# Kernel optimization log

Measured on AMD Instinct MI355X. Metric: run time of the kernel, lower is better.

The kernel has to match this reference:

```python
import jax, jax.numpy as jnp
import numpy as np

B, S, D, H = 4, 2048, 1024, 16
DH = D // H
SCALE = float(np.sqrt(DH))


def setup_inputs() -> dict:
    key = jax.random.key(0)
    ks = jax.random.split(key, 5)
    std = 1.0 / np.sqrt(D)
    return {
        "x": jax.random.normal(ks[0], (B, S, D), dtype=jnp.float32),
        "Wq": jax.random.normal(ks[1], (D, D), dtype=jnp.float32) * std,
        "bq": jnp.zeros((D,), dtype=jnp.float32),
        "Wk": jax.random.normal(ks[2], (D, D), dtype=jnp.float32) * std,
        "bk": jnp.zeros((D,), dtype=jnp.float32),
        "Wv": jax.random.normal(ks[3], (D, D), dtype=jnp.float32) * std,
        "bv": jnp.zeros((D,), dtype=jnp.float32),
        "Wo": jax.random.normal(ks[4], (D, D), dtype=jnp.float32) * std,
        "bo": jnp.zeros((D,), dtype=jnp.float32),
        "padding_mask": jnp.ones((B, S), dtype=jnp.int32),
    }


def reference(x, Wq, bq, Wk, bk, Wv, bv, Wo, bo, padding_mask):
    b, s, d = x.shape
    # QKV projections, split heads -> [b, h, s, dh]
    q = (x @ Wq + bq).reshape(b, s, H, DH).transpose(0, 2, 1, 3)
    k = (x @ Wk + bk).reshape(b, s, H, DH).transpose(0, 2, 1, 3)
    v = (x @ Wv + bv).reshape(b, s, H, DH).transpose(0, 2, 1, 3)
    # scaled scores [b, h, s, s]
    scores = jnp.einsum('bhqd,bhkd->bhqk', q, k) / SCALE
    neg_inf = jnp.float32(-jnp.inf)
    causal = jnp.tril(jnp.ones((s, s), dtype=bool))  # [s, s]
    scores = jnp.where(causal[None, None, :, :], scores, neg_inf)
    pad = (padding_mask != 0)[:, None, None, :]  # [b,1,1,s] on key axis
    scores = jnp.where(pad, scores, neg_inf)
    weights = jax.nn.softmax(scores, axis=-1)
    weights = jnp.nan_to_num(weights, nan=0.0)  # fully-masked rows -> 0
    # dropout is identity in eval / p=0
    attended = jnp.einsum('bhqk,bhkd->bhqd', weights, v)
    attended = attended.transpose(0, 2, 1, 3).reshape(b, s, d)
    return attended @ Wo + bo
```

## Files before the change

### kernel.cpp

```cpp
#include <hip/hip_runtime.h>
#include <hip/hip_bf16.h>

#define B_   4
#define S_   2048
#define D_   1024
#define H_   16
#define DH_  64
#define M_   (B_ * S_)

typedef __attribute__((ext_vector_type(8))) short  bfrag8;
typedef __attribute__((ext_vector_type(4))) float  facc4;
typedef unsigned short u16;
typedef unsigned long long u64;

__device__ __forceinline__ u16 f2bf(float f) {
    union { __hip_bfloat16 h; u16 u; } c;
    c.h = __float2bfloat16(f);
    return c.u;
}

__device__ __forceinline__ u16 bfr(float f) {
    unsigned b = __float_as_uint(f);
    return (u16)((b + 0x7FFFu + ((b >> 16) & 1u)) >> 16);
}

__device__ __forceinline__ void gl_lds16(const u16* g, u16* l) {
    __builtin_amdgcn_global_load_lds((const __attribute__((address_space(1))) void*)g,
                                     (__attribute__((address_space(3))) void*)l,
                                     16, 0, 0);
}

__global__ __launch_bounds__(256) void cvt_x(const float* __restrict__ x,
                                             u16* __restrict__ o, int n) {
    int i = (blockIdx.x * 256 + threadIdx.x) * 4;
    if (i >= n) return;
    float4 v = *(const float4*)(x + i);
    ushort4 r;
    r.x = f2bf(v.x); r.y = f2bf(v.y); r.z = f2bf(v.z); r.w = f2bf(v.w);
    *(ushort4*)(o + i) = r;
}

__global__ __launch_bounds__(256) void cvt_wt(const float* __restrict__ w0, const float* __restrict__ w1,
                                              const float* __restrict__ w2, const float* __restrict__ w3,
                                              u16* __restrict__ o0, u16* __restrict__ o1,
                                              u16* __restrict__ o2, u16* __restrict__ o3) {
    const float* w; u16* o;
    switch (blockIdx.z) {
        case 0: w = w0; o = o0; break;
        case 1: w = w1; o = o1; break;
        case 2: w = w2; o = o2; break;
        default: w = w3; o = o3; break;
    }
    __shared__ u16 t[32][33];
    int kb = blockIdx.x * 32, nb = blockIdx.y * 32;
    int c = threadIdx.x & 31, r0 = threadIdx.x >> 5;
#pragma unroll
    for (int i = 0; i < 4; i++) {
        int r = r0 + 8 * i;
        t[r][c] = f2bf(w[(kb + r) * D_ + nb + c]);
    }
    __syncthreads();
#pragma unroll
    for (int i = 0; i < 4; i++) {
        int r = r0 + 8 * i;
        o[(nb + r) * D_ + kb + c] = t[c][r];
    }
}

__global__ __launch_bounds__(64) void pack_pm(const int* __restrict__ pm,
                                              unsigned* __restrict__ pmw) {
    int b = blockIdx.x, lane = threadIdx.x;
#pragma unroll
    for (int j = 0; j < 32; ++j) {
        u64 m = __ballot(pm[b * S_ + j * 64 + lane] != 0);
        if (lane == 0) {
            pmw[b * 64 + 2 * j]     = (unsigned)m;
            pmw[b * 64 + 2 * j + 1] = (unsigned)(m >> 32);
        }
    }
}

__device__ __forceinline__ void gemm_body(const u16* __restrict__ A,
                                          const u16* __restrict__ BT,
                                          const float* __restrict__ bias,
                                          void* __restrict__ Cout, int mode, float scale,
                                          u16* As, u16* Bs) {
    int tid = threadIdx.x;
    int nb = blockIdx.x * 128, mb = blockIdx.y * 128;
    int w = tid >> 6, lane = tid & 63, quad = lane >> 4, l16 = lane & 15;
    int wm = (w >> 1) * 64, wn = (w & 1) * 64;

    int c0 = tid, c1 = tid + 256;
    int row0 = c0 >> 2, row1 = c1 >> 2;
    int sw0 = (c0 & 3) ^ ((row0 >> 2) & 3);
    int sw1 = (c1 & 3) ^ ((row1 >> 2) & 3);
    const u16* Ag0 = A + (mb + row0) * D_ + sw0 * 8;
    const u16* Ag1 = A + (mb + row1) * D_ + sw1 * 8;
    const u16* Bg0 = BT + (nb + row0) * D_ + sw0 * 8;
    const u16* Bg1 = BT + (nb + row1) * D_ + sw1 * 8;
    u16* Al0 = As + c0 * 8; u16* Al1 = As + c1 * 8;
    u16* Bl0 = Bs + c0 * 8; u16* Bl1 = Bs + c1 * 8;

    int swr = (l16 >> 2) & 3;

    facc4 acc[4][4] = {};
    for (int kk = 0; kk < D_; kk += 32) {
        __syncthreads();
        gl_lds16(Ag0 + kk, Al0);
        gl_lds16(Ag1 + kk, Al1);
        gl_lds16(Bg0 + kk, Bl0);
        gl_lds16(Bg1 + kk, Bl1);
        __syncthreads();

        bfrag8 af[4], bf[4];
#pragma unroll
        for (int mt = 0; mt < 4; ++mt)
            af[mt] = *(const bfrag8*)(As + (wm + mt * 16 + l16) * 32 + ((quad ^ swr) << 3));
#pragma unroll
        for (int nt = 0; nt < 4; ++nt)
            bf[nt] = *(const bfrag8*)(Bs + (wn + nt * 16 + l16) * 32 + ((quad ^ swr) << 3));
#pragma unroll
        for (int mt = 0; mt < 4; ++mt)
#pragma unroll
            for (int nt = 0; nt < 4; ++nt)
                acc[mt][nt] = __builtin_amdgcn_mfma_f32_16x16x32_bf16(af[mt], bf[nt], acc[mt][nt], 0, 0, 0);
    }

#pragma unroll
    for (int mt = 0; mt < 4; ++mt) {
        int m_base = mb + wm + mt * 16 + quad * 4;
#pragma unroll
        for (int nt = 0; nt < 4; ++nt) {
            int n = nb + wn + nt * 16 + l16;
            float bv = bias[n];
            int h = n >> 6, dd = n & 63;
#pragma unroll
            for (int r = 0; r < 4; ++r) {
                int m = m_base + r;
                float v = (acc[mt][nt][r] + bv) * scale;
                int bi = m >> 11, s = m & (S_ - 1);
                if (mode == 0) {
                    ((u16*)Cout)[(((bi * H_ + h) * S_) + s) * DH_ + dd] = bfr(v);
                } else if (mode == 1) {
                    ((u16*)Cout)[(((bi * H_ + h) * DH_) + dd) * S_ + s] = bfr(v);
                } else {
                    ((float*)Cout)[(size_t)m * D_ + n] = v;
                }
            }
        }
    }
}

#define CE_Q 0.18033688011112042f

__global__ __launch_bounds__(256) void gemm_qkv(const u16* __restrict__ A,
                                                const u16* __restrict__ WTq, const float* __restrict__ bq, u16* __restrict__ Qb,
                                                const u16* __restrict__ WTk, const float* __restrict__ bk, u16* __restrict__ Kb,
                                                const u16* __restrict__ WTv, const float* __restrict__ bv, u16* __restrict__ VTb) {
    __shared__ u16 As[128 * 32];
    __shared__ u16 Bs[128 * 32];
    switch (blockIdx.z) {
        case 0: gemm_body(A, WTq, bq, Qb, 0, CE_Q, As, Bs); break;
        case 1: gemm_body(A, WTk, bk, Kb, 0, 1.0f, As, Bs); break;
        default: gemm_body(A, WTv, bv, VTb, 1, 1.0f, As, Bs); break;
    }
}

__global__ __launch_bounds__(256) void gemm_o(const u16* __restrict__ A,
                                              const u16* __restrict__ WTo, const float* __restrict__ bo,
                                              float* __restrict__ out) {
    __shared__ u16 As[128 * 32];
    __shared__ u16 Bs[128 * 32];
    gemm_body(A, WTo, bo, out, 2, 1.0f, As, Bs);
}

__device__ __forceinline__ void soft_pv(const float* p, float& lp, facc4* oaccq,
                                        const bfrag8* vf, int a0, int a1, bool qlo) {
    float rs = 0.f;
    unsigned pk[4];
#pragma unroll
    for (int j = 0; j < 4; ++j) {
        float e0 = exp2f(p[2 * j]);
        float e1 = exp2f(p[2 * j + 1]);
        rs += e0; rs += e1;
        pk[j] = __builtin_amdgcn_perm(__float_as_uint(e1), __float_as_uint(e0), 0x07060302u);
    }
    lp += rs;
    union { unsigned d[4]; bfrag8 v; } pb;
    {
        unsigned lo, hi;
        lo = __builtin_amdgcn_ds_bpermute(a0, (int)pk[0]);
        hi = __builtin_amdgcn_ds_bpermute(a0, (int)pk[2]);
        pb.d[0] = qlo ? lo : hi;
        lo = __builtin_amdgcn_ds_bpermute(a0, (int)pk[1]);
        hi = __builtin_amdgcn_ds_bpermute(a0, (int)pk[3]);
        pb.d[1] = qlo ? lo : hi;
        lo = __builtin_amdgcn_ds_bpermute(a1, (int)pk[0]);
        hi = __builtin_amdgcn_ds_bpermute(a1, (int)pk[2]);
        pb.d[2] = qlo ? lo : hi;
        lo = __builtin_amdgcn_ds_bpermute(a1, (int)pk[1]);
        hi = __builtin_amdgcn_ds_bpermute(a1, (int)pk[3]);
        pb.d[3] = qlo ? lo : hi;
    }
    __builtin_amdgcn_s_setprio(1);
#pragma unroll
    for (int dt = 0; dt < 4; ++dt)
        oaccq[dt] = __builtin_amdgcn_mfma_f32_16x16x32_bf16(vf[dt], pb.v, oaccq[dt], 0, 0, 0);
    __builtin_amdgcn_s_setprio(0);
}

__global__ __launch_bounds__(256, 4) void attn(const u16* __restrict__ Q,
                                               const u16* __restrict__ K,
                                               const u16* __restrict__ VT,
                                               const unsigned* __restrict__ pmw,
                                               u16* __restrict__ Aout) {
    __shared__ __attribute__((aligned(16))) u16 Ks[32 * 64];
    __shared__ __attribute__((aligned(16))) u16 Vs[64 * 32];

    int tid = threadIdx.x, w = tid >> 6, lane = tid & 63;
    int quad = lane >> 4, l16 = lane & 15;

    int lid = blockIdx.x;
    int bh  = (lid & 7) * 8 + ((lid >> 3) & 7);
    int ci  = 15 - (lid >> 6);
    int b = bh >> 4, h = bh & 15;

    int qbase = ci * 128;
    int qw = qbase + w * 32;
    int tmax = (qbase >> 5) + 3;

    const u16* Qp = Q + (size_t)(b * H_ + h) * S_ * DH_;
    const u16* Kp = K + (size_t)(b * H_ + h) * S_ * DH_;
    const u16* Vp = VT + (size_t)(b * H_ + h) * DH_ * S_;
    const unsigned* pmb = pmw + b * 64;
    u16* Ao = Aout + (size_t)b * S_ * D_ + h * DH_;

    int krow = tid >> 3, ku = tid & 7;
    const u16* Kg = Kp + krow * DH_ + ((ku ^ (krow & 7)) * 8);
    u16* Kl = Ks + tid * 8;
    int vrow = tid >> 2, vu = tid & 3;
    const u16* Vg = Vp + vrow * S_ + ((vu ^ (vrow & 3)) * 8);
    u16* Vl = Vs + tid * 8;

    int k7 = l16 & 7, v3 = l16 & 3;

    int a0 = ((((2 * quad) & 3) * 16 + l16) << 2);
    int a1 = ((((2 * quad + 1) & 3) * 16 + l16) << 2);
    bool qlo = quad < 2;

    bfrag8 qf[2][2];
#pragma unroll
    for (int qt = 0; qt < 2; ++qt)
#pragma unroll
        for (int cc = 0; cc < 2; ++cc)
            qf[qt][cc] = *(const bfrag8*)(Qp + (qw + qt * 16 + l16) * DH_ + cc * 32 + quad * 8);

    facc4 oacc[2][4] = {};
    float lp[2] = {0.f, 0.f};

    for (int t = 0; t <= tmax; ++t) {
        int k0 = t * 32;
        __syncthreads();
        gl_lds16(Kg + k0 * DH_, Kl);
        gl_lds16(Vg + k0, Vl);
        __syncthreads();

        bfrag8 kf00 = *(const bfrag8*)(Ks + (l16 * 8        + ((quad)     ^ k7)) * 8);
        bfrag8 kf01 = *(const bfrag8*)(Ks + (l16 * 8        + ((quad + 4) ^ k7)) * 8);
        bfrag8 kf10 = *(const bfrag8*)(Ks + ((l16 + 16) * 8 + ((quad)     ^ k7)) * 8);
        bfrag8 kf11 = *(const bfrag8*)(Ks + ((l16 + 16) * 8 + ((quad + 4) ^ k7)) * 8);
        bfrag8 vf[4];
#pragma unroll
        for (int dt = 0; dt < 4; ++dt)
            vf[dt] = *(const bfrag8*)(Vs + ((dt * 16 + l16) * 4 + (quad ^ v3)) * 8);

        unsigned vm = pmb[t];

        facc4 st[2][2] = {};
        __builtin_amdgcn_s_setprio(1);
#pragma unroll
        for (int qt = 0; qt < 2; ++qt) {
            st[qt][0] = __builtin_amdgcn_mfma_f32_16x16x32_bf16(kf00, qf[qt][0], st[qt][0], 0, 0, 0);
            st[qt][0] = __builtin_amdgcn_mfma_f32_16x16x32_bf16(kf01, qf[qt][1], st[qt][0], 0, 0, 0);
            st[qt][1] = __builtin_amdgcn_mfma_f32_16x16x32_bf16(kf10, qf[qt][0], st[qt][1], 0, 0, 0);
            st[qt][1] = __builtin_amdgcn_mfma_f32_16x16x32_bf16(kf11, qf[qt][1], st[qt][1], 0, 0, 0);
        }
        __builtin_amdgcn_s_setprio(0);

        if (vm == 0xffffffffu && k0 + 31 < qw) {
#pragma unroll
            for (int qt = 0; qt < 2; ++qt) {
                float p[8];
#pragma unroll
                for (int kt = 0; kt < 2; ++kt)
#pragma unroll
                    for (int r = 0; r < 4; ++r) p[kt * 4 + r] = st[qt][kt][r];
                soft_pv(p, lp[qt], oacc[qt], vf, a0, a1, qlo);
            }
        } else {
#pragma unroll
            for (int qt = 0; qt < 2; ++qt) {
                int q0 = qw + qt * 16;
                float p[8];
#pragma unroll
                for (int kt = 0; kt < 2; ++kt)
#pragma unroll
                    for (int r = 0; r < 4; ++r) {
                        int kl = kt * 16 + quad * 4 + r;
                        bool ok = ((vm >> kl) & 1u) && (k0 + kl <= q0 + l16);
                        p[kt * 4 + r] = ok ? st[qt][kt][r] : -1e30f;
                    }
                soft_pv(p, lp[qt], oacc[qt], vf, a0, a1, qlo);
            }
        }
    }

#pragma unroll
    for (int qt = 0; qt < 2; ++qt) {
        float l = lp[qt];
        l += __shfl_xor(l, 16);
        l += __shfl_xor(l, 32);
        float linv = (l > 0.f) ? 1.f / l : 0.f;
        size_t qoff = (size_t)(qw + qt * 16 + l16) * D_;
#pragma unroll
        for (int dt = 0; dt < 4; ++dt) {
            union { u16 hh[4]; u64 q; } pk4;
#pragma unroll
            for (int r = 0; r < 4; ++r) pk4.hh[r] = bfr(oacc[qt][dt][r] * linv);
            *(u64*)(Ao + qoff + dt * 16 + quad * 4) = pk4.q;
        }
    }
}

extern "C" void kernel_launch(void* const* d_in, const int* in_sizes, int n_in,
                              void* d_out, int out_size, void* d_ws, size_t ws_size,
                              hipStream_t stream) {
    const float* x  = (const float*)d_in[0];
    const float* Wq = (const float*)d_in[1];
    const float* bq = (const float*)d_in[2];
    const float* Wk = (const float*)d_in[3];
    const float* bk = (const float*)d_in[4];
    const float* Wv = (const float*)d_in[5];
    const float* bv = (const float*)d_in[6];
    const float* Wo = (const float*)d_in[7];
    const float* bo = (const float*)d_in[8];
    const int*   pm = (const int*)d_in[9];
    float* out = (float*)d_out;

    char* ws = (char*)d_ws;
    const size_t SZ_XD = (size_t)M_ * D_ * 2;
    const size_t SZ_W  = (size_t)D_ * D_ * 2;
    u16* X16 = (u16*)ws;
    u16* WTq = (u16*)(ws + SZ_XD);
    u16* WTk = (u16*)(ws + SZ_XD + SZ_W);
    u16* WTv = (u16*)(ws + SZ_XD + 2 * SZ_W);
    u16* WTo = (u16*)(ws + SZ_XD + 3 * SZ_W);
    u16* Qb  = (u16*)(ws + SZ_XD + 4 * SZ_W);
    u16* Kb  = (u16*)(ws + 2 * SZ_XD + 4 * SZ_W);
    u16* VTb = (u16*)(ws + 3 * SZ_XD + 4 * SZ_W);
    u16* Att = X16;
    unsigned* PMW = (unsigned*)WTq;

    cvt_x<<<(M_ * D_) / (256 * 4), 256, 0, stream>>>(x, X16, M_ * D_);
    cvt_wt<<<dim3(D_ / 32, D_ / 32, 4), 256, 0, stream>>>(Wq, Wk, Wv, Wo, WTq, WTk, WTv, WTo);

    gemm_qkv<<<dim3(D_ / 128, M_ / 128, 3), 256, 0, stream>>>(X16, WTq, bq, Qb, WTk, bk, Kb, WTv, bv, VTb);

    pack_pm<<<4, 64, 0, stream>>>(pm, PMW);

    attn<<<dim3(1024), 256, 0, stream>>>(Qb, Kb, VTb, PMW, Att);

    gemm_o<<<dim3(D_ / 128, M_ / 128), 256, 0, stream>>>(Att, WTo, bo, out);
}
```

Before: 310.5 us.

## Double-buffer GEMM LDS tiles with 256x128 blocks and BK=64

Rewrites the projection GEMM body to use 512-thread blocks computing 256x128 tiles with a K-step of 64. LDS is double-buffered, so global-to-LDS loads for the next K tile are issued while MFMAs run on the current one, with one barrier per iteration instead of two. The swizzle is widened to 8 chunks to fit the 64-wide rows, and MFMA sections are wrapped in setprio. It uses about 96KB of LDS per block, which limits occupancy, and halves the number of blocks along M.

```diff
diff --git a/kernel.cpp b/kernel.cpp
--- a/kernel.cpp
+++ b/kernel.cpp
@@ -80,50 +80,77 @@
     }
 }
 
-__device__ __forceinline__ void gemm_body(const u16* __restrict__ A,
-                                          const u16* __restrict__ BT,
-                                          const float* __restrict__ bias,
-                                          void* __restrict__ Cout, int mode, float scale,
-                                          u16* As, u16* Bs) {
+#define ABUF_ (256 * 64)
+#define TBUF_ ((256 + 128) * 64)
+
+__device__ __forceinline__ void gemm_body256(const u16* __restrict__ A,
+                                             const u16* __restrict__ BT,
+                                             const float* __restrict__ bias,
+                                             void* __restrict__ Cout, int mode, float scale,
+                                             u16* S) {
     int tid = threadIdx.x;
-    int nb = blockIdx.x * 128, mb = blockIdx.y * 128;
+    int nb = blockIdx.x * 128, mb = blockIdx.y * 256;
     int w = tid >> 6, lane = tid & 63, quad = lane >> 4, l16 = lane & 15;
     int wm = (w >> 1) * 64, wn = (w & 1) * 64;
-
-    int c0 = tid, c1 = tid + 256;
-    int row0 = c0 >> 2, row1 = c1 >> 2;
-    int sw0 = (c0 & 3) ^ ((row0 >> 2) & 3);
-    int sw1 = (c1 & 3) ^ ((row1 >> 2) & 3);
-    const u16* Ag0 = A + (mb + row0) * D_ + sw0 * 8;
-    const u16* Ag1 = A + (mb + row1) * D_ + sw1 * 8;
-    const u16* Bg0 = BT + (nb + row0) * D_ + sw0 * 8;
-    const u16* Bg1 = BT + (nb + row1) * D_ + sw1 * 8;
-    u16* Al0 = As + c0 * 8; u16* Al1 = As + c1 * 8;
-    u16* Bl0 = Bs + c0 * 8; u16* Bl1 = Bs + c1 * 8;
-
-    int swr = (l16 >> 2) & 3;
+    int x7 = l16 & 7;
+
+    const u16* Aga[4]; const u16* Bga[2];
+#pragma unroll
+    for (int i = 0; i < 4; ++i) {
+        int idx = i * 512 + tid, row = idx >> 3;
+        int lu = (idx & 7) ^ (row & 7);
+        Aga[i] = A + (size_t)(mb + row) * D_ + lu * 8;
+    }
+#pragma unroll
+    for (int i = 0; i < 2; ++i) {
+        int idx = i * 512 + tid, row = idx >> 3;
+        int lu = (idx & 7) ^ (row & 7);
+        Bga[i] = BT + (size_t)(nb + row) * D_ + lu * 8;
+    }
 
     facc4 acc[4][4] = {};
-    for (int kk = 0; kk < D_; kk += 32) {
-        __syncthreads();
-        gl_lds16(Ag0 + kk, Al0);
-        gl_lds16(Ag1 + kk, Al1);
-        gl_lds16(Bg0 + kk, Bl0);
-        gl_lds16(Bg1 + kk, Bl1);
-        __syncthreads();
-
-        bfrag8 af[4], bf[4];
-#pragma unroll
-        for (int mt = 0; mt < 4; ++mt)
-            af[mt] = *(const bfrag8*)(As + (wm + mt * 16 + l16) * 32 + ((quad ^ swr) << 3));
-#pragma unroll
-        for (int nt = 0; nt < 4; ++nt)
-            bf[nt] = *(const bfrag8*)(Bs + (wn + nt * 16 + l16) * 32 + ((quad ^ swr) << 3));
-#pragma unroll
-        for (int mt = 0; mt < 4; ++mt)
+
+#pragma unroll
+    for (int i = 0; i < 4; ++i) gl_lds16(Aga[i], S + (i * 512 + tid) * 8);
+#pragma unroll
+    for (int i = 0; i < 2; ++i) gl_lds16(Bga[i], S + ABUF_ + (i * 512 + tid) * 8);
+    asm volatile("s_waitcnt vmcnt(0)" ::: "memory");
+    __builtin_amdgcn_sched_barrier(0);
+    __builtin_amdgcn_s_barrier();
+    __builtin_amdgcn_sched_barrier(0);
+
+    for (int kt = 0; kt < 16; ++kt) {
+        u16* Cb = S + (kt & 1) * TBUF_;
+        u16* Nb = S + ((kt & 1) ^ 1) * TBUF_;
+        if (kt < 15) {
+            int ko = (kt + 1) * 64;
+#pragma unroll
+            for (int i = 0; i < 4; ++i) gl_lds16(Aga[i] + ko, Nb + (i * 512 + tid) * 8);
+#pragma unroll
+            for (int i = 0; i < 2; ++i) gl_lds16(Bga[i] + ko, Nb + ABUF_ + (i * 512 + tid) * 8);
+        }
+#pragma unroll
+        for (int k2 = 0; k2 < 2; ++k2) {
+            int pu = ((k2 * 4 + quad) ^ x7) * 8;
+            bfrag8 af[4], bf[4];
+#pragma unroll
+            for (int mt = 0; mt < 4; ++mt)
+                af[mt] = *(const bfrag8*)(Cb + (wm + mt * 16 + l16) * 64 + pu);
 #pragma unroll
             for (int nt = 0; nt < 4; ++nt)
-                acc[mt][nt] = __builtin_amdgcn_mfma_f32_16x16x32_bf16(af[mt], bf[nt], acc[mt][nt], 0, 0, 0);
+                bf[nt] = *(const bfrag8*)(Cb + ABUF_ + (wn + nt * 16 + l16) * 64 + pu);
+            __builtin_amdgcn_s_setprio(1);
+#pragma unroll
+            for (int mt = 0; mt < 4; ++mt)
+#pragma unroll
+                for (int nt = 0; nt < 4; ++nt)
+                    acc[mt][nt] = __builtin_amdgcn_mfma_f32_16x16x32_bf16(af[mt], bf[nt], acc[mt][nt], 0, 0, 0);
+            __builtin_amdgcn_s_setprio(0);
+        }
+        asm volatile("s_waitcnt vmcnt(0)" ::: "memory");
+        __builtin_amdgcn_sched_barrier(0);
+        __builtin_amdgcn_s_barrier();
+        __builtin_amdgcn_sched_barrier(0);
     }
 
 #pragma unroll
@@ -153,25 +180,23 @@
 
 #define CE_Q 0.18033688011112042f
 
-__global__ __launch_bounds__(256) void gemm_qkv(const u16* __restrict__ A,
+__global__ __launch_bounds__(512, 2) void gemm_qkv(const u16* __restrict__ A,
                                                 const u16* __restrict__ WTq, const float* __restrict__ bq, u16* __restrict__ Qb,
                                                 const u16* __restrict__ WTk, const float* __restrict__ bk, u16* __restrict__ Kb,
                                                 const u16* __restrict__ WTv, const float* __restrict__ bv, u16* __restrict__ VTb) {
-    __shared__ u16 As[128 * 32];
-    __shared__ u16 Bs[128 * 32];
+    __shared__ __attribute__((aligned(16))) u16 Sh[2 * TBUF_];
     switch (blockIdx.z) {
-        case 0: gemm_body(A, WTq, bq, Qb, 0, CE_Q, As, Bs); break;
-        case 1: gemm_body(A, WTk, bk, Kb, 0, 1.0f, As, Bs); break;
-        default: gemm_body(A, WTv, bv, VTb, 1, 1.0f, As, Bs); break;
-    }
-}
-
-__global__ __launch_bounds__(256) void gemm_o(const u16* __restrict__ A,
+        case 0: gemm_body256(A, WTq, bq, Qb, 0, CE_Q, Sh); break;
+        case 1: gemm_body256(A, WTk, bk, Kb, 0, 1.0f, Sh); break;
+        default: gemm_body256(A, WTv, bv, VTb, 1, 1.0f, Sh); break;
+    }
+}
+
+__global__ __launch_bounds__(512, 2) void gemm_o(const u16* __restrict__ A,
                                               const u16* __restrict__ WTo, const float* __restrict__ bo,
                                               float* __restrict__ out) {
-    __shared__ u16 As[128 * 32];
-    __shared__ u16 Bs[128 * 32];
-    gemm_body(A, WTo, bo, out, 2, 1.0f, As, Bs);
+    __shared__ __attribute__((aligned(16))) u16 Sh[2 * TBUF_];
+    gemm_body256(A, WTo, bo, out, 2, 1.0f, Sh);
 }
 
 __device__ __forceinline__ void soft_pv(const float* p, float& lp, facc4* oaccq,
@@ -364,11 +389,11 @@
     cvt_x<<<(M_ * D_) / (256 * 4), 256, 0, stream>>>(x, X16, M_ * D_);
     cvt_wt<<<dim3(D_ / 32, D_ / 32, 4), 256, 0, stream>>>(Wq, Wk, Wv, Wo, WTq, WTk, WTv, WTo);
 
-    gemm_qkv<<<dim3(D_ / 128, M_ / 128, 3), 256, 0, stream>>>(X16, WTq, bq, Qb, WTk, bk, Kb, WTv, bv, VTb);
+    gemm_qkv<<<dim3(D_ / 128, M_ / 256, 3), 512, 0, stream>>>(X16, WTq, bq, Qb, WTk, bk, Kb, WTv, bv, VTb);
 
     pack_pm<<<4, 64, 0, stream>>>(pm, PMW);
 
     attn<<<dim3(1024), 256, 0, stream>>>(Qb, Kb, VTb, PMW, Att);
 
-    gemm_o<<<dim3(D_ / 128, M_ / 128), 256, 0, stream>>>(Att, WTo, bo, out);
-}
+    gemm_o<<<dim3(D_ / 128, M_ / 256), 512, 0, stream>>>(Att, WTo, bo, out);
+}
```

After: 296.9 us. -4.4%, faster.
